# Kernel optimization log

Measured on AMD Instinct MI355X. Metric: run time of the kernel, lower is better.

## Reference

```python
import jax, jax.numpy as jnp
import numpy as np

D_MODEL = 128
N_HEAD = 6
D_HEAD = D_MODEL // N_HEAD  # 21
D_CAT = N_HEAD * D_HEAD     # 126 (note: != d_model, matches torch source)
D_FF = 4 * D_MODEL
EPS = 1e-5


def setup_inputs() -> dict:
    key = jax.random.key(0)
    ks = jax.random.split(key, 12)
    B, T = 512, 128
    s = 0.02
    return {
        "x":  jax.random.normal(ks[0], (B, T, D_MODEL), dtype=jnp.float32),
        "Wq": jax.random.normal(ks[1], (N_HEAD, D_MODEL, D_HEAD), dtype=jnp.float32) * s,
        "Wk": jax.random.normal(ks[2], (N_HEAD, D_MODEL, D_HEAD), dtype=jnp.float32) * s,
        "Wv": jax.random.normal(ks[3], (N_HEAD, D_MODEL, D_HEAD), dtype=jnp.float32) * s,
        "Wo": jax.random.normal(ks[4], (D_CAT, D_MODEL), dtype=jnp.float32) * s,
        "bo": jnp.zeros((D_MODEL,), dtype=jnp.float32),
        "W1": jax.random.normal(ks[5], (D_MODEL, D_FF), dtype=jnp.float32) * s,
        "b1": jnp.zeros((D_FF,), dtype=jnp.float32),
        "W2": jax.random.normal(ks[6], (D_FF, D_MODEL), dtype=jnp.float32) * s,
        "b2": jnp.zeros((D_MODEL,), dtype=jnp.float32),
        "g1": jnp.ones((D_MODEL,), dtype=jnp.float32),
        "beta1": jnp.zeros((D_MODEL,), dtype=jnp.float32),
        "g2": jnp.ones((D_MODEL,), dtype=jnp.float32),
        "beta2": jnp.zeros((D_MODEL,), dtype=jnp.float32),
    }


def _layernorm(x, g, b):
    mu = jnp.mean(x, axis=-1, keepdims=True)
    var = jnp.mean(jnp.square(x - mu), axis=-1, keepdims=True)
    return (x - mu) * jax.lax.rsqrt(var + EPS) * g + b


def reference(x, Wq, Wk, Wv, Wo, bo, W1, b1, W2, b2, g1, beta1, g2, beta2):
    B, T, _ = x.shape
    # --- masked multi-head self-attention on ln1(x) (pre-norm), dropout = eval/identity ---
    h = _layernorm(x, g1, beta1)
    q = jnp.einsum('btd,hde->bhte', h, Wq)
    k = jnp.einsum('btd,hde->bhte', h, Wk)
    v = jnp.einsum('btd,hde->bhte', h, Wv)
    scores = jnp.einsum('bhte,bhse->bhts', q, k) / jnp.sqrt(jnp.float32(D_HEAD))
    causal = jnp.tril(jnp.ones((T, T), dtype=bool))  # tril buffer, T x T
    scores = jnp.where(causal, scores, jnp.float32(-jnp.inf))
    a = jax.nn.softmax(scores, axis=-1)
    o = jnp.einsum('bhts,bhse->bhte', a, v)
    o = o.transpose(0, 2, 1, 3).reshape(B, T, D_CAT)  # concat heads -> 126
    x = x + (o @ Wo + bo)
    # --- feed-forward on ln2(x) ---
    h2 = _layernorm(x, g2, beta2)
    ff = jax.nn.relu(h2 @ W1 + b1) @ W2 + b2
    return x + ff
```

## Files before the change

### kernel.cpp

```cpp
#include <hip/hip_runtime.h>
#include <math.h>

typedef short short8 __attribute__((ext_vector_type(8)));
typedef float f32x4 __attribute__((ext_vector_type(4)));

constexpr int B_ = 512, T_ = 128, D_ = 128, H_ = 6, E_ = 21, DC_ = 126, F_ = 512;
constexpr float EPS_ = 1e-5f;

__device__ __forceinline__ short f2bf(float f) {
    unsigned u = __float_as_uint(f);
    u = (u + 0x7FFFu + ((u >> 16) & 1u)) >> 16;
    return (short)u;
}
__device__ __forceinline__ unsigned pk2(float lo, float hi) {
    return (unsigned)(unsigned short)f2bf(lo) | ((unsigned)(unsigned short)f2bf(hi) << 16);
}
__device__ __forceinline__ f32x4 mfma16(short8 a, short8 b, f32x4 c) {
    return __builtin_amdgcn_mfma_f32_16x16x32_bf16(a, b, c, 0, 0, 0);
}

__global__ __launch_bounds__(256) void prep_kernel(
    const float* __restrict__ Wq, const float* __restrict__ Wk, const float* __restrict__ Wv,
    const float* __restrict__ Wo, const float* __restrict__ W1, const float* __restrict__ W2,
    short* __restrict__ WcatT, short* __restrict__ W1T, short* __restrict__ W2T,
    short* __restrict__ WoT) {
    int idx = blockIdx.x * 256 + threadIdx.x;
    if (idx < 73728) {
        int n = idx >> 7, k = idx & 127;
        int w = (n >= 384) ? 2 : (n >= 192 ? 1 : 0);
        int rem = n - w * 192;
        int hd = rem >> 5, e = rem & 31;
        float v = 0.f;
        if (e < 21) {
            const float* src = (w == 0) ? Wq : (w == 1) ? Wk : Wv;
            v = src[(hd * 128 + k) * 21 + e];
        }
        WcatT[idx] = f2bf(v);
    } else if (idx < 139264) {
        int i = idx - 73728;
        int j = i >> 7, d = i & 127;
        W1T[i] = f2bf(W1[d * 512 + j]);
    } else if (idx < 204800) {
        int i = idx - 139264;
        int d = i >> 9, j = i & 511;
        W2T[i] = f2bf(W2[j * 128 + d]);
    } else if (idx < 221184) {
        int i = idx - 204800;
        int d = i >> 7, c = i & 127;
        WoT[i] = f2bf(c < 126 ? Wo[c * 128 + d] : 0.f);
    }
}

__global__ __launch_bounds__(512) void qkv_kernel(
    const float* __restrict__ x, const float* __restrict__ g1, const float* __restrict__ be1,
    const short* __restrict__ WcatT,
    short* __restrict__ Qg, short* __restrict__ Kg, short* __restrict__ VTg) {
    __shared__ __align__(16) short hA[T_ * D_];
    int b = blockIdx.x, tid = threadIdx.x;
    const f32x4 fzero = {0.f, 0.f, 0.f, 0.f};
    {
        int r = tid >> 2, q = tid & 3;
        const float* xr = x + ((size_t)b * T_ + r) * D_ + q * 32;
        float vals[32];
        float sum = 0.f, sq = 0.f;
        #pragma unroll
        for (int i = 0; i < 8; ++i) {
            f32x4 v4 = *(const f32x4*)(xr + i * 4);
            #pragma unroll
            for (int j = 0; j < 4; ++j) { float vv = v4[j]; vals[i*4+j] = vv; sum += vv; sq += vv*vv; }
        }
        sum += __shfl_xor(sum, 1); sum += __shfl_xor(sum, 2);
        sq  += __shfl_xor(sq, 1);  sq  += __shfl_xor(sq, 2);
        float mu = sum * (1.f / 128.f);
        float rs = rsqrtf(sq * (1.f / 128.f) - mu * mu + EPS_);
        char* hb = (char*)hA;
        #pragma unroll
        for (int cc = 0; cc < 4; ++cc) {
            short8 pk;
            #pragma unroll
            for (int j = 0; j < 8; ++j) {
                int d0 = q * 32 + cc * 8 + j;
                pk[j] = f2bf((vals[cc*8+j] - mu) * rs * g1[d0] + be1[d0]);
            }
            int byte = (r * 256 + q * 64 + cc * 16) ^ ((r & 7) << 4);
            *(short8*)(hb + byte) = pk;
        }
    }
    __syncthreads();
    int lane = tid & 63, wid = tid >> 6;
    int wm = wid >> 2, wn = wid & 3;
    int rlo = lane & 15, khi = lane >> 4;
    f32x4 acc[4][9];
    #pragma unroll
    for (int m = 0; m < 4; ++m)
        #pragma unroll
        for (int j = 0; j < 9; ++j) acc[m][j] = fzero;
    const char* hb = (const char*)hA;
    #pragma unroll
    for (int ks = 0; ks < 4; ++ks) {
        short8 hfr[4];
        #pragma unroll
        for (int m = 0; m < 4; ++m) {
            int row = (wm * 4 + m) * 16 + rlo;
            hfr[m] = *(const short8*)(hb + ((row * 256 + ks * 64 + khi * 16) ^ ((row & 7) << 4)));
        }
        #pragma unroll
        for (int j = 0; j < 9; ++j) {
            int nt = wn * 9 + j;
            short8 wf = *(const short8*)(WcatT + (size_t)(nt * 16 + rlo) * 128 + ks * 32 + khi * 8);
            if (nt < 24) {
                #pragma unroll
                for (int m = 0; m < 4; ++m) acc[m][j] = mfma16(wf, hfr[m], acc[m][j]);
            } else {
                #pragma unroll
                for (int m = 0; m < 4; ++m) acc[m][j] = mfma16(hfr[m], wf, acc[m][j]);
            }
        }
    }
    #pragma unroll
    for (int j = 0; j < 9; ++j) {
        int nt = wn * 9 + j;
        if (nt < 24) {
            int ng = nt * 16 + khi * 4;
            int w = (ng >= 192) ? 1 : 0;
            int hd = (ng >> 5) - w * 6;
            int e32 = ng & 31;
            short* dst = (w ? Kg : Qg) + (((size_t)b * 6 + hd) * 128) * 32 + e32;
            #pragma unroll
            for (int m = 0; m < 4; ++m) {
                int t = (wm * 4 + m) * 16 + rlo;
                uint2 pv;
                pv.x = pk2(acc[m][j][0], acc[m][j][1]);
                pv.y = pk2(acc[m][j][2], acc[m][j][3]);
                *(uint2*)(dst + (size_t)t * 32) = pv;
            }
        } else {
            int ng = nt * 16 + rlo;
            int hd = (ng >> 5) - 12;
            int e32 = ng & 31;
            short* dst = VTg + (((size_t)b * 6 + hd) * 32 + e32) * 128;
            #pragma unroll
            for (int m = 0; m < 4; ++m) {
                int t0 = (wm * 4 + m) * 16 + khi * 4;
                uint2 pv;
                pv.x = pk2(acc[m][j][0], acc[m][j][1]);
                pv.y = pk2(acc[m][j][2], acc[m][j][3]);
                *(uint2*)(dst + t0) = pv;
            }
        }
    }
}

__global__ __launch_bounds__(256) void attn_kernel(
    const short* __restrict__ Qg, const short* __restrict__ Kg, const short* __restrict__ VTg,
    short* __restrict__ Obf) {
    __shared__ __align__(16) short Ks[T_ * 32];
    __shared__ __align__(16) short VTs[32 * T_];
    __shared__ __align__(16) short Ps[T_ * T_];
    int h = blockIdx.x, b = blockIdx.y, tid = threadIdx.x;
    size_t bh = (size_t)b * 6 + h;
    const f32x4 fzero = {0.f, 0.f, 0.f, 0.f};
    {
        char* kb = (char*)Ks;
        const short* Ksrc = Kg + bh * (128 * 32);
        #pragma unroll
        for (int c = tid; c < 512; c += 256) {
            int r = c >> 2, cc = c & 3;
            *(short8*)(kb + ((r * 64 + cc * 16) ^ ((r & 3) << 4))) =
                *(const short8*)(Ksrc + r * 32 + cc * 8);
        }
        char* vb = (char*)VTs;
        const short* Vsrc = VTg + bh * (32 * 128);
        #pragma unroll
        for (int c = tid; c < 512; c += 256) {
            int e = c >> 4, cc = c & 15;
            *(short8*)(vb + ((e * 256 + cc * 16) ^ ((e & 7) << 4))) =
                *(const short8*)(Vsrc + e * 128 + cc * 8);
        }
    }
    __syncthreads();
    int lane = tid & 63, wid = tid >> 6;
    int rlo = lane & 15, khi = lane >> 4;
    const float s2 = 0.31482188f;
    const char* kb = (const char*)Ks;
    const char* vb = (const char*)VTs;
    char* pb = (char*)Ps;
    #pragma unroll
    for (int pass = 0; pass < 2; ++pass) {
        int Mt = (pass == 0) ? wid : 7 - wid;
        int t = Mt * 16 + rlo;
        short8 qf = *(const short8*)(Qg + (bh * 128 + t) * 32 + khi * 8);
        f32x4 sacc[8];
        #pragma unroll
        for (int St = 0; St < 8; ++St) {
            sacc[St] = fzero;
            if (St <= Mt) {
                int srow = St * 16 + rlo;
                short8 kf = *(const short8*)(kb + ((srow * 64 + khi * 16) ^ ((srow & 3) << 4)));
                sacc[St] = mfma16(kf, qf, sacc[St]);
            }
        }
        float m = -3e38f;
        #pragma unroll
        for (int St = 0; St < 8; ++St)
            #pragma unroll
            for (int reg = 0; reg < 4; ++reg) {
                int s = St * 16 + khi * 4 + reg;
                float v = (s <= t) ? sacc[St][reg] * s2 : -3e38f;
                sacc[St][reg] = v;
                m = fmaxf(m, v);
            }
        m = fmaxf(m, __shfl_xor(m, 16));
        m = fmaxf(m, __shfl_xor(m, 32));
        float sum = 0.f;
        #pragma unroll
        for (int St = 0; St < 8; ++St)
            #pragma unroll
            for (int reg = 0; reg < 4; ++reg) {
                float p = exp2f(sacc[St][reg] - m);
                sacc[St][reg] = p;
                sum += p;
            }
        sum += __shfl_xor(sum, 16);
        sum += __shfl_xor(sum, 32);
        float inv = 1.f / sum;
        #pragma unroll
        for (int St = 0; St < 8; ++St) {
            uint2 pv;
            pv.x = pk2(sacc[St][0] * inv, sacc[St][1] * inv);
            pv.y = pk2(sacc[St][2] * inv, sacc[St][3] * inv);
            *(uint2*)(pb + ((t * 256 + St * 32 + khi * 8) ^ ((t & 7) << 4))) = pv;
        }
        f32x4 o0 = fzero, o1 = fzero;
        int kmax = Mt >> 1;
        for (int ks = 0; ks <= kmax; ++ks) {
            int kof = ks * 64 + khi * 16;
            int arow = Mt * 16 + rlo;
            short8 pa = *(const short8*)(pb + ((arow * 256 + kof) ^ ((arow & 7) << 4)));
            short8 b0 = *(const short8*)(vb + ((rlo * 256 + kof) ^ ((rlo & 7) << 4)));
            short8 b1v = *(const short8*)(vb + (((16 + rlo) * 256 + kof) ^ (((16 + rlo) & 7) << 4)));
            o0 = mfma16(pa, b0, o0);
            o1 = mfma16(pa, b1v, o1);
        }
        #pragma unroll
        for (int reg = 0; reg < 4; ++reg) {
            int t2 = Mt * 16 + khi * 4 + reg;
            Obf[((size_t)b * 128 + t2) * 128 + h * 21 + rlo] = f2bf(o0[reg]);
            if (rlo < 5)
                Obf[((size_t)b * 128 + t2) * 128 + h * 21 + 16 + rlo] = f2bf(o1[reg]);
        }
    }
}

__global__ __launch_bounds__(256) void proj_kernel(
    const float* __restrict__ x, const short* __restrict__ Obf, const short* __restrict__ WoT,
    const float* __restrict__ bo, float* __restrict__ out) {
    __shared__ __align__(16) short Os[64 * 128];
    int r0 = blockIdx.x * 64, tid = threadIdx.x;
    const f32x4 fzero = {0.f, 0.f, 0.f, 0.f};
    char* ob = (char*)Os;
    for (int c = tid; c < 1024; c += 256) {
        int r = c >> 4, cc = c & 15;
        short8 v = *(const short8*)(Obf + (size_t)(r0 + r) * 128 + cc * 8);
        if (cc == 15) { v[6] = 0; v[7] = 0; }
        int byte = (r * 256 + cc * 16) ^ ((r & 7) << 4);
        *(short8*)(ob + byte) = v;
    }
    __syncthreads();
    int lane = tid & 63, mt = tid >> 6;
    int rlo = lane & 15, khi = lane >> 4;
    #pragma unroll
    for (int nt = 0; nt < 8; ++nt) {
        int d = nt * 16 + rlo;
        f32x4 acc = fzero;
        #pragma unroll
        for (int ks = 0; ks < 4; ++ks) {
            int arow = mt * 16 + rlo;
            short8 a = *(const short8*)(ob + ((arow * 256 + ks * 64 + khi * 16) ^ ((arow & 7) << 4)));
            short8 bf = *(const short8*)(WoT + d * 128 + ks * 32 + khi * 8);
            acc = mfma16(a, bf, acc);
        }
        float bod = bo[d];
        #pragma unroll
        for (int reg = 0; reg < 4; ++reg) {
            int row = r0 + mt * 16 + khi * 4 + reg;
            out[(size_t)row * 128 + d] = x[(size_t)row * 128 + d] + bod + acc[reg];
        }
    }
}

__global__ __launch_bounds__(256, 2) void ff_kernel(
    float* __restrict__ out, const float* __restrict__ g2, const float* __restrict__ be2,
    const short* __restrict__ W1T, const float* __restrict__ b1,
    const short* __restrict__ W2T, const float* __restrict__ b2) {
    __shared__ __align__(16) short Hs[64 * 128];
    __shared__ __align__(16) short Fs[64 * 512];
    int tid = threadIdx.x;
    int lane = tid & 63, wid = tid >> 6;
    int rlo = lane & 15, khi = lane >> 4;
    int rowbase = blockIdx.x * 64;
    const f32x4 fzero = {0.f, 0.f, 0.f, 0.f};
    {
        int rl = lane >> 2, q = lane & 3;
        int r = wid * 16 + rl;
        const float* xr = out + (size_t)(rowbase + r) * D_ + q * 32;
        float vals[32];
        float sum = 0.f, sq = 0.f;
        #pragma unroll
        for (int i = 0; i < 8; ++i) {
            f32x4 v4 = *(const f32x4*)(xr + i * 4);
            #pragma unroll
            for (int j = 0; j < 4; ++j) { float vv = v4[j]; vals[i*4+j] = vv; sum += vv; sq += vv*vv; }
        }
        sum += __shfl_xor(sum, 1); sum += __shfl_xor(sum, 2);
        sq  += __shfl_xor(sq, 1);  sq  += __shfl_xor(sq, 2);
        float mu = sum * (1.f / 128.f);
        float rs = rsqrtf(sq * (1.f / 128.f) - mu * mu + EPS_);
        char* hb = (char*)Hs;
        #pragma unroll
        for (int cc = 0; cc < 4; ++cc) {
            short8 pk;
            #pragma unroll
            for (int j = 0; j < 8; ++j) {
                int d0 = q * 32 + cc * 8 + j;
                pk[j] = f2bf((vals[cc*8+j] - mu) * rs * g2[d0] + be2[d0]);
            }
            int byte = (r * 256 + q * 64 + cc * 16) ^ ((r & 7) << 4);
            *(short8*)(hb + byte) = pk;
        }
    }
    __syncthreads();
    short8 hfr[4][4];
    {
        const char* hb = (const char*)Hs;
        #pragma unroll
        for (int mt = 0; mt < 4; ++mt)
            #pragma unroll
            for (int kk = 0; kk < 4; ++kk) {
                int t = mt * 16 + rlo;
                hfr[mt][kk] = *(const short8*)(hb + ((t * 256 + kk * 64 + khi * 16) ^ ((t & 7) << 4)));
            }
    }
    {
        const short* W1w = W1T + (size_t)(wid * 128) * 128;
        char* fb = (char*)Fs;
        #pragma unroll 2
        for (int jt = 0; jt < 8; ++jt) {
            f32x4 fa[4];
            #pragma unroll
            for (int mt = 0; mt < 4; ++mt) fa[mt] = fzero;
            #pragma unroll
            for (int kk = 0; kk < 4; ++kk) {
                short8 wa = *(const short8*)(W1w + (size_t)(jt * 16 + rlo) * 128 + kk * 32 + khi * 8);
                #pragma unroll
                for (int mt = 0; mt < 4; ++mt) fa[mt] = mfma16(wa, hfr[mt][kk], fa[mt]);
            }
            f32x4 bq = *(const f32x4*)(b1 + wid * 128 + jt * 16 + khi * 4);
            #pragma unroll
            for (int mt = 0; mt < 4; ++mt) {
                float v0 = fmaxf(fa[mt][0] + bq[0], 0.f);
                float v1 = fmaxf(fa[mt][1] + bq[1], 0.f);
                float v2 = fmaxf(fa[mt][2] + bq[2], 0.f);
                float v3 = fmaxf(fa[mt][3] + bq[3], 0.f);
                uint2 w;
                w.x = pk2(v0, v1);
                w.y = pk2(v2, v3);
                int t = mt * 16 + rlo;
                int byte = (t * 1024 + wid * 256 + jt * 32 + khi * 8) ^ ((t & 7) << 4);
                *(uint2*)(fb + byte) = w;
            }
        }
    }
    __syncthreads();
    f32x4 oa[4][2];
    #pragma unroll
    for (int mt = 0; mt < 4; ++mt) { oa[mt][0] = fzero; oa[mt][1] = fzero; }
    {
        const char* fb = (const char*)Fs;
        const short* W2w = W2T + (size_t)(wid * 32) * 512;
        #pragma unroll 4
        for (int ks = 0; ks < 16; ++ks) {
            short8 af[4];
            #pragma unroll
            for (int mt = 0; mt < 4; ++mt) {
                int t = mt * 16 + rlo;
                af[mt] = *(const short8*)(fb + ((t * 1024 + ks * 64 + khi * 16) ^ ((t & 7) << 4)));
            }
            #pragma unroll
            for (int nd = 0; nd < 2; ++nd) {
                short8 wf = *(const short8*)(W2w + (size_t)(nd * 16 + rlo) * 512 + ks * 32 + khi * 8);
                #pragma unroll
                for (int mt = 0; mt < 4; ++mt) oa[mt][nd] = mfma16(af[mt], wf, oa[mt][nd]);
            }
        }
    }
    #pragma unroll
    for (int nd = 0; nd < 2; ++nd) {
        int d = wid * 32 + nd * 16 + rlo;
        float b2d = b2[d];
        #pragma unroll
        for (int mt = 0; mt < 4; ++mt) {
            #pragma unroll
            for (int reg = 0; reg < 4; ++reg) {
                int row = rowbase + mt * 16 + khi * 4 + reg;
                size_t gi = (size_t)row * D_ + d;
                out[gi] = out[gi] + b2d + oa[mt][nd][reg];
            }
        }
    }
}

extern "C" void kernel_launch(void* const* d_in, const int* in_sizes, int n_in,
                              void* d_out, int out_size, void* d_ws, size_t ws_size,
                              hipStream_t stream) {
    const float* x   = (const float*)d_in[0];
    const float* Wq  = (const float*)d_in[1];
    const float* Wk  = (const float*)d_in[2];
    const float* Wv  = (const float*)d_in[3];
    const float* Wo  = (const float*)d_in[4];
    const float* bo  = (const float*)d_in[5];
    const float* W1  = (const float*)d_in[6];
    const float* b1  = (const float*)d_in[7];
    const float* W2  = (const float*)d_in[8];
    const float* b2  = (const float*)d_in[9];
    const float* g1  = (const float*)d_in[10];
    const float* be1 = (const float*)d_in[11];
    const float* g2  = (const float*)d_in[12];
    const float* be2 = (const float*)d_in[13];
    float* out = (float*)d_out;

    char* wsb = (char*)d_ws;
    short* WcatT = (short*)(wsb);
    short* W1T   = (short*)(wsb + 147456);
    short* W2T   = (short*)(wsb + 278528);
    short* WoT   = (short*)(wsb + 409600);
    short* Qg    = (short*)(wsb + 442368);
    short* Kg    = (short*)(wsb + 25608192);
    short* VTg   = (short*)(wsb + 50774016);
    short* Obf   = (short*)(wsb + 75939840);

    prep_kernel<<<864, 256, 0, stream>>>(Wq, Wk, Wv, Wo, W1, W2, WcatT, W1T, W2T, WoT);
    qkv_kernel<<<512, 512, 0, stream>>>(x, g1, be1, WcatT, Qg, Kg, VTg);
    attn_kernel<<<dim3(6, 512), 256, 0, stream>>>(Qg, Kg, VTg, Obf);
    proj_kernel<<<1024, 256, 0, stream>>>(x, Obf, WoT, bo, out);
    ff_kernel<<<1024, 256, 0, stream>>>(out, g2, be2, W1T, b1, W2T, b2);
}
```

Before: 283.5 us.

## Fuse QKV projection, attention and output projection into one per-batch kernel

Merges the QKV, attention and projection kernels into a single kernel per batch element. Q, K, V^T and the concatenated head outputs stay in shared memory, and heads are processed sequentially with block-wide syncs. This removes the large bf16 intermediate round trips through global memory and two kernel launches. In exchange, LDS use grows to about 120KB per block, which limits occupancy to one 512-thread block per CU and serializes heads within a block.

```diff
diff --git a/kernel.cpp b/kernel.cpp
--- a/kernel.cpp
+++ b/kernel.cpp
@@ -51,11 +51,16 @@
     }
 }
 
-__global__ __launch_bounds__(512) void qkv_kernel(
+__global__ __launch_bounds__(512, 2) void mega_kernel(
     const float* __restrict__ x, const float* __restrict__ g1, const float* __restrict__ be1,
-    const short* __restrict__ WcatT,
-    short* __restrict__ Qg, short* __restrict__ Kg, short* __restrict__ VTg) {
+    const short* __restrict__ WcatT, const short* __restrict__ WoT,
+    const float* __restrict__ bo, float* __restrict__ out) {
     __shared__ __align__(16) short hA[T_ * D_];
+    __shared__ __align__(16) short Qh[T_ * 32];
+    __shared__ __align__(16) short Kh[T_ * 32];
+    __shared__ __align__(16) short VTh[32 * T_];
+    __shared__ __align__(16) short Ps[T_ * T_];
+    __shared__ __align__(16) short Os[T_ * T_];
     int b = blockIdx.x, tid = threadIdx.x;
     const f32x4 fzero = {0.f, 0.f, 0.f, 0.f};
     {
@@ -85,206 +90,153 @@
             int byte = (r * 256 + q * 64 + cc * 16) ^ ((r & 7) << 4);
             *(short8*)(hb + byte) = pk;
         }
-    }
-    __syncthreads();
-    int lane = tid & 63, wid = tid >> 6;
-    int wm = wid >> 2, wn = wid & 3;
-    int rlo = lane & 15, khi = lane >> 4;
-    f32x4 acc[4][9];
-    #pragma unroll
-    for (int m = 0; m < 4; ++m)
-        #pragma unroll
-        for (int j = 0; j < 9; ++j) acc[m][j] = fzero;
-    const char* hb = (const char*)hA;
-    #pragma unroll
-    for (int ks = 0; ks < 4; ++ks) {
-        short8 hfr[4];
-        #pragma unroll
-        for (int m = 0; m < 4; ++m) {
-            int row = (wm * 4 + m) * 16 + rlo;
-            hfr[m] = *(const short8*)(hb + ((row * 256 + ks * 64 + khi * 16) ^ ((row & 7) << 4)));
-        }
-        #pragma unroll
-        for (int j = 0; j < 9; ++j) {
-            int nt = wn * 9 + j;
-            short8 wf = *(const short8*)(WcatT + (size_t)(nt * 16 + rlo) * 128 + ks * 32 + khi * 8);
-            if (nt < 24) {
-                #pragma unroll
-                for (int m = 0; m < 4; ++m) acc[m][j] = mfma16(wf, hfr[m], acc[m][j]);
-            } else {
-                #pragma unroll
-                for (int m = 0; m < 4; ++m) acc[m][j] = mfma16(hfr[m], wf, acc[m][j]);
-            }
-        }
-    }
-    #pragma unroll
-    for (int j = 0; j < 9; ++j) {
-        int nt = wn * 9 + j;
-        if (nt < 24) {
-            int ng = nt * 16 + khi * 4;
-            int w = (ng >= 192) ? 1 : 0;
-            int hd = (ng >> 5) - w * 6;
-            int e32 = ng & 31;
-            short* dst = (w ? Kg : Qg) + (((size_t)b * 6 + hd) * 128) * 32 + e32;
-            #pragma unroll
-            for (int m = 0; m < 4; ++m) {
-                int t = (wm * 4 + m) * 16 + rlo;
-                uint2 pv;
-                pv.x = pk2(acc[m][j][0], acc[m][j][1]);
-                pv.y = pk2(acc[m][j][2], acc[m][j][3]);
-                *(uint2*)(dst + (size_t)t * 32) = pv;
-            }
-        } else {
-            int ng = nt * 16 + rlo;
-            int hd = (ng >> 5) - 12;
-            int e32 = ng & 31;
-            short* dst = VTg + (((size_t)b * 6 + hd) * 32 + e32) * 128;
-            #pragma unroll
-            for (int m = 0; m < 4; ++m) {
-                int t0 = (wm * 4 + m) * 16 + khi * 4;
-                uint2 pv;
-                pv.x = pk2(acc[m][j][0], acc[m][j][1]);
-                pv.y = pk2(acc[m][j][2], acc[m][j][3]);
-                *(uint2*)(dst + t0) = pv;
-            }
-        }
-    }
-}
-
-__global__ __launch_bounds__(256) void attn_kernel(
-    const short* __restrict__ Qg, const short* __restrict__ Kg, const short* __restrict__ VTg,
-    short* __restrict__ Obf) {
-    __shared__ __align__(16) short Ks[T_ * 32];
-    __shared__ __align__(16) short VTs[32 * T_];
-    __shared__ __align__(16) short Ps[T_ * T_];
-    int h = blockIdx.x, b = blockIdx.y, tid = threadIdx.x;
-    size_t bh = (size_t)b * 6 + h;
-    const f32x4 fzero = {0.f, 0.f, 0.f, 0.f};
-    {
-        char* kb = (char*)Ks;
-        const short* Ksrc = Kg + bh * (128 * 32);
-        #pragma unroll
-        for (int c = tid; c < 512; c += 256) {
-            int r = c >> 2, cc = c & 3;
-            *(short8*)(kb + ((r * 64 + cc * 16) ^ ((r & 3) << 4))) =
-                *(const short8*)(Ksrc + r * 32 + cc * 8);
-        }
-        char* vb = (char*)VTs;
-        const short* Vsrc = VTg + bh * (32 * 128);
-        #pragma unroll
-        for (int c = tid; c < 512; c += 256) {
-            int e = c >> 4, cc = c & 15;
-            *(short8*)(vb + ((e * 256 + cc * 16) ^ ((e & 7) << 4))) =
-                *(const short8*)(Vsrc + e * 128 + cc * 8);
-        }
+        short8 z = {0,0,0,0,0,0,0,0};
+        char* ob = (char*)Os;
+        #pragma unroll
+        for (int i = tid; i < 2048; i += 512) *(short8*)(ob + i * 16) = z;
     }
     __syncthreads();
     int lane = tid & 63, wid = tid >> 6;
     int rlo = lane & 15, khi = lane >> 4;
+    short8 hfr[4];
+    {
+        const char* hb = (const char*)hA;
+        int row = wid * 16 + rlo;
+        #pragma unroll
+        for (int kk = 0; kk < 4; ++kk)
+            hfr[kk] = *(const short8*)(hb + ((row * 256 + kk * 64 + khi * 16) ^ ((row & 7) << 4)));
+    }
     const float s2 = 0.31482188f;
-    const char* kb = (const char*)Ks;
-    const char* vb = (const char*)VTs;
+    char* qhb = (char*)Qh;
+    char* khb = (char*)Kh;
+    char* vtb = (char*)VTh;
     char* pb = (char*)Ps;
-    #pragma unroll
-    for (int pass = 0; pass < 2; ++pass) {
-        int Mt = (pass == 0) ? wid : 7 - wid;
-        int t = Mt * 16 + rlo;
-        short8 qf = *(const short8*)(Qg + (bh * 128 + t) * 32 + khi * 8);
-        f32x4 sacc[8];
-        #pragma unroll
-        for (int St = 0; St < 8; ++St) {
-            sacc[St] = fzero;
-            if (St <= Mt) {
-                int srow = St * 16 + rlo;
-                short8 kf = *(const short8*)(kb + ((srow * 64 + khi * 16) ^ ((srow & 3) << 4)));
-                sacc[St] = mfma16(kf, qf, sacc[St]);
-            }
-        }
-        float m = -3e38f;
-        #pragma unroll
-        for (int St = 0; St < 8; ++St)
+    char* osb = (char*)Os;
+    for (int h = 0; h < 6; ++h) {
+        const short* Wqb = WcatT + (size_t)(h * 32) * 128;
+        const short* Wkb = WcatT + (size_t)(192 + h * 32) * 128;
+        const short* Wvb = WcatT + (size_t)(384 + h * 32) * 128;
+        #pragma unroll
+        for (int nq = 0; nq < 2; ++nq) {
+            f32x4 qa = fzero, ka = fzero;
+            #pragma unroll
+            for (int ks = 0; ks < 4; ++ks) {
+                short8 wfq = *(const short8*)(Wqb + (size_t)(nq * 16 + rlo) * 128 + ks * 32 + khi * 8);
+                short8 wfk = *(const short8*)(Wkb + (size_t)(nq * 16 + rlo) * 128 + ks * 32 + khi * 8);
+                qa = mfma16(wfq, hfr[ks], qa);
+                ka = mfma16(wfk, hfr[ks], ka);
+            }
+            int t = wid * 16 + rlo;
+            int byte = (t * 64 + (nq * 16 + khi * 4) * 2) ^ ((t & 3) << 4);
+            uint2 qv, kv;
+            qv.x = pk2(qa[0], qa[1]); qv.y = pk2(qa[2], qa[3]);
+            kv.x = pk2(ka[0], ka[1]); kv.y = pk2(ka[2], ka[3]);
+            *(uint2*)(qhb + byte) = qv;
+            *(uint2*)(khb + byte) = kv;
+        }
+        #pragma unroll
+        for (int nv = 0; nv < 2; ++nv) {
+            f32x4 va = fzero;
+            #pragma unroll
+            for (int ks = 0; ks < 4; ++ks) {
+                short8 wfv = *(const short8*)(Wvb + (size_t)(nv * 16 + rlo) * 128 + ks * 32 + khi * 8);
+                va = mfma16(hfr[ks], wfv, va);
+            }
+            int e = nv * 16 + rlo;
+            int t0 = wid * 16 + khi * 4;
+            int byte = (e * 256 + t0 * 2) ^ ((e & 7) << 4);
+            uint2 vv;
+            vv.x = pk2(va[0], va[1]); vv.y = pk2(va[2], va[3]);
+            *(uint2*)(vtb + byte) = vv;
+        }
+        __syncthreads();
+        #pragma unroll
+        for (int pass = 0; pass < 2; ++pass) {
+            int Mt = (pass == 0) ? wid : 7 - wid;
+            int t = Mt * 16 + rlo;
+            short8 qf = *(const short8*)(qhb + ((t * 64 + khi * 16) ^ ((t & 3) << 4)));
+            f32x4 sacc[8];
+            #pragma unroll
+            for (int St = 0; St < 8; ++St) {
+                sacc[St] = fzero;
+                if (St <= Mt) {
+                    int srow = St * 16 + rlo;
+                    short8 kf = *(const short8*)(khb + ((srow * 64 + khi * 16) ^ ((srow & 3) << 4)));
+                    sacc[St] = mfma16(kf, qf, sacc[St]);
+                }
+            }
+            float m = -3e38f;
+            #pragma unroll
+            for (int St = 0; St < 8; ++St)
+                #pragma unroll
+                for (int reg = 0; reg < 4; ++reg) {
+                    int s = St * 16 + khi * 4 + reg;
+                    float v = (s <= t) ? sacc[St][reg] * s2 : -3e38f;
+                    sacc[St][reg] = v;
+                    m = fmaxf(m, v);
+                }
+            m = fmaxf(m, __shfl_xor(m, 16));
+            m = fmaxf(m, __shfl_xor(m, 32));
+            float sum = 0.f;
+            #pragma unroll
+            for (int St = 0; St < 8; ++St)
+                #pragma unroll
+                for (int reg = 0; reg < 4; ++reg) {
+                    float p = exp2f(sacc[St][reg] - m);
+                    sacc[St][reg] = p;
+                    sum += p;
+                }
+            sum += __shfl_xor(sum, 16);
+            sum += __shfl_xor(sum, 32);
+            float inv = 1.f / sum;
+            #pragma unroll
+            for (int St = 0; St < 8; ++St) {
+                uint2 pv;
+                pv.x = pk2(sacc[St][0] * inv, sacc[St][1] * inv);
+                pv.y = pk2(sacc[St][2] * inv, sacc[St][3] * inv);
+                *(uint2*)(pb + ((t * 256 + St * 32 + khi * 8) ^ ((t & 7) << 4))) = pv;
+            }
+            f32x4 o0 = fzero, o1 = fzero;
+            int kmax = Mt >> 1;
+            for (int ks = 0; ks <= kmax; ++ks) {
+                int kof = ks * 64 + khi * 16;
+                int arow = Mt * 16 + rlo;
+                short8 pa = *(const short8*)(pb + ((arow * 256 + kof) ^ ((arow & 7) << 4)));
+                short8 b0 = *(const short8*)(vtb + ((rlo * 256 + kof) ^ ((rlo & 7) << 4)));
+                short8 b1v = *(const short8*)(vtb + (((16 + rlo) * 256 + kof) ^ (((16 + rlo) & 7) << 4)));
+                o0 = mfma16(pa, b0, o0);
+                o1 = mfma16(pa, b1v, o1);
+            }
             #pragma unroll
             for (int reg = 0; reg < 4; ++reg) {
-                int s = St * 16 + khi * 4 + reg;
-                float v = (s <= t) ? sacc[St][reg] * s2 : -3e38f;
-                sacc[St][reg] = v;
-                m = fmaxf(m, v);
-            }
-        m = fmaxf(m, __shfl_xor(m, 16));
-        m = fmaxf(m, __shfl_xor(m, 32));
-        float sum = 0.f;
-        #pragma unroll
-        for (int St = 0; St < 8; ++St)
-            #pragma unroll
-            for (int reg = 0; reg < 4; ++reg) {
-                float p = exp2f(sacc[St][reg] - m);
-                sacc[St][reg] = p;
-                sum += p;
-            }
-        sum += __shfl_xor(sum, 16);
-        sum += __shfl_xor(sum, 32);
-        float inv = 1.f / sum;
-        #pragma unroll
-        for (int St = 0; St < 8; ++St) {
-            uint2 pv;
-            pv.x = pk2(sacc[St][0] * inv, sacc[St][1] * inv);
-            pv.y = pk2(sacc[St][2] * inv, sacc[St][3] * inv);
-            *(uint2*)(pb + ((t * 256 + St * 32 + khi * 8) ^ ((t & 7) << 4))) = pv;
-        }
-        f32x4 o0 = fzero, o1 = fzero;
-        int kmax = Mt >> 1;
-        for (int ks = 0; ks <= kmax; ++ks) {
-            int kof = ks * 64 + khi * 16;
-            int arow = Mt * 16 + rlo;
-            short8 pa = *(const short8*)(pb + ((arow * 256 + kof) ^ ((arow & 7) << 4)));
-            short8 b0 = *(const short8*)(vb + ((rlo * 256 + kof) ^ ((rlo & 7) << 4)));
-            short8 b1v = *(const short8*)(vb + (((16 + rlo) * 256 + kof) ^ (((16 + rlo) & 7) << 4)));
-            o0 = mfma16(pa, b0, o0);
-            o1 = mfma16(pa, b1v, o1);
-        }
-        #pragma unroll
-        for (int reg = 0; reg < 4; ++reg) {
-            int t2 = Mt * 16 + khi * 4 + reg;
-            Obf[((size_t)b * 128 + t2) * 128 + h * 21 + rlo] = f2bf(o0[reg]);
-            if (rlo < 5)
-                Obf[((size_t)b * 128 + t2) * 128 + h * 21 + 16 + rlo] = f2bf(o1[reg]);
-        }
-    }
-}
-
-__global__ __launch_bounds__(256) void proj_kernel(
-    const float* __restrict__ x, const short* __restrict__ Obf, const short* __restrict__ WoT,
-    const float* __restrict__ bo, float* __restrict__ out) {
-    __shared__ __align__(16) short Os[64 * 128];
-    int r0 = blockIdx.x * 64, tid = threadIdx.x;
-    const f32x4 fzero = {0.f, 0.f, 0.f, 0.f};
-    char* ob = (char*)Os;
-    for (int c = tid; c < 1024; c += 256) {
-        int r = c >> 4, cc = c & 15;
-        short8 v = *(const short8*)(Obf + (size_t)(r0 + r) * 128 + cc * 8);
-        if (cc == 15) { v[6] = 0; v[7] = 0; }
-        int byte = (r * 256 + cc * 16) ^ ((r & 7) << 4);
-        *(short8*)(ob + byte) = v;
-    }
-    __syncthreads();
-    int lane = tid & 63, mt = tid >> 6;
-    int rlo = lane & 15, khi = lane >> 4;
+                int t2 = Mt * 16 + khi * 4 + reg;
+                int col = h * 21 + rlo;
+                *(short*)(osb + ((t2 * 256 + col * 2) ^ ((t2 & 7) << 4))) = f2bf(o0[reg]);
+                if (rlo < 5) {
+                    int col1 = h * 21 + 16 + rlo;
+                    *(short*)(osb + ((t2 * 256 + col1 * 2) ^ ((t2 & 7) << 4))) = f2bf(o1[reg]);
+                }
+            }
+        }
+        __syncthreads();
+    }
     #pragma unroll
     for (int nt = 0; nt < 8; ++nt) {
         int d = nt * 16 + rlo;
         f32x4 acc = fzero;
         #pragma unroll
         for (int ks = 0; ks < 4; ++ks) {
-            int arow = mt * 16 + rlo;
-            short8 a = *(const short8*)(ob + ((arow * 256 + ks * 64 + khi * 16) ^ ((arow & 7) << 4)));
-            short8 bf = *(const short8*)(WoT + d * 128 + ks * 32 + khi * 8);
+            int arow = wid * 16 + rlo;
+            short8 a = *(const short8*)(osb + ((arow * 256 + ks * 64 + khi * 16) ^ ((arow & 7) << 4)));
+            short8 bf = *(const short8*)(WoT + (size_t)d * 128 + ks * 32 + khi * 8);
             acc = mfma16(a, bf, acc);
         }
         float bod = bo[d];
         #pragma unroll
         for (int reg = 0; reg < 4; ++reg) {
-            int row = r0 + mt * 16 + khi * 4 + reg;
-            out[(size_t)row * 128 + d] = x[(size_t)row * 128 + d] + bod + acc[reg];
+            int row = wid * 16 + khi * 4 + reg;
+            size_t gi = ((size_t)b * T_ + row) * D_ + d;
+            out[gi] = x[gi] + bod + acc[reg];
         }
     }
 }
@@ -434,14 +386,8 @@
     short* W1T   = (short*)(wsb + 147456);
     short* W2T   = (short*)(wsb + 278528);
     short* WoT   = (short*)(wsb + 409600);
-    short* Qg    = (short*)(wsb + 442368);
-    short* Kg    = (short*)(wsb + 25608192);
-    short* VTg   = (short*)(wsb + 50774016);
-    short* Obf   = (short*)(wsb + 75939840);
 
     prep_kernel<<<864, 256, 0, stream>>>(Wq, Wk, Wv, Wo, W1, W2, WcatT, W1T, W2T, WoT);
-    qkv_kernel<<<512, 512, 0, stream>>>(x, g1, be1, WcatT, Qg, Kg, VTg);
-    attn_kernel<<<dim3(6, 512), 256, 0, stream>>>(Qg, Kg, VTg, Obf);
-    proj_kernel<<<1024, 256, 0, stream>>>(x, Obf, WoT, bo, out);
+    mega_kernel<<<512, 512, 0, stream>>>(x, g1, be1, WcatT, WoT, bo, out);
     ff_kernel<<<1024, 256, 0, stream>>>(out, g2, be2, W1T, b1, W2T, b2);
 }
```

Measured after the change: 312.5 us. 1.1x slower.

## Split QKV kernel into 32-row blocks and skip padded head-dim traffic

Applied to the files above, without the earlier changes.

The QKV projection kernel now launches four 256-thread blocks per batch, each covering 32 rows, instead of one 512-thread block per batch. Each warp preloads its LDS fragments once and handles 9 output column tiles for 2 row tiles. The QKV kernel also stops writing the padded head-dim lanes (e 24..31), and the attention kernel stops reading them, filling zeros in LDS instead. The aim is more blocks for better occupancy and less global memory traffic, at the cost of reading the weight fragments more times overall.

```diff
diff --git a/kernel.cpp b/kernel.cpp
--- a/kernel.cpp
+++ b/kernel.cpp
@@ -51,101 +51,111 @@
     }
 }
 
-__global__ __launch_bounds__(512) void qkv_kernel(
+__global__ __launch_bounds__(256) void qkv_kernel(
     const float* __restrict__ x, const float* __restrict__ g1, const float* __restrict__ be1,
     const short* __restrict__ WcatT,
     short* __restrict__ Qg, short* __restrict__ Kg, short* __restrict__ VTg) {
-    __shared__ __align__(16) short hA[T_ * D_];
-    int b = blockIdx.x, tid = threadIdx.x;
+    __shared__ __align__(16) short hA[32 * 128];
+    int bid = blockIdx.x;
+    int b = bid >> 2, r0 = (bid & 3) * 32;
+    int tid = threadIdx.x;
     const f32x4 fzero = {0.f, 0.f, 0.f, 0.f};
     {
-        int r = tid >> 2, q = tid & 3;
-        const float* xr = x + ((size_t)b * T_ + r) * D_ + q * 32;
-        float vals[32];
+        int r = tid >> 3, q = tid & 7;
+        const float* xr = x + ((size_t)b * T_ + r0 + r) * D_ + q * 16;
+        float vals[16];
         float sum = 0.f, sq = 0.f;
         #pragma unroll
-        for (int i = 0; i < 8; ++i) {
+        for (int i = 0; i < 4; ++i) {
             f32x4 v4 = *(const f32x4*)(xr + i * 4);
             #pragma unroll
             for (int j = 0; j < 4; ++j) { float vv = v4[j]; vals[i*4+j] = vv; sum += vv; sq += vv*vv; }
         }
-        sum += __shfl_xor(sum, 1); sum += __shfl_xor(sum, 2);
-        sq  += __shfl_xor(sq, 1);  sq  += __shfl_xor(sq, 2);
+        sum += __shfl_xor(sum, 1); sum += __shfl_xor(sum, 2); sum += __shfl_xor(sum, 4);
+        sq  += __shfl_xor(sq, 1);  sq  += __shfl_xor(sq, 2);  sq  += __shfl_xor(sq, 4);
         float mu = sum * (1.f / 128.f);
         float rs = rsqrtf(sq * (1.f / 128.f) - mu * mu + EPS_);
         char* hb = (char*)hA;
         #pragma unroll
-        for (int cc = 0; cc < 4; ++cc) {
+        for (int cc = 0; cc < 2; ++cc) {
             short8 pk;
             #pragma unroll
             for (int j = 0; j < 8; ++j) {
-                int d0 = q * 32 + cc * 8 + j;
+                int d0 = q * 16 + cc * 8 + j;
                 pk[j] = f2bf((vals[cc*8+j] - mu) * rs * g1[d0] + be1[d0]);
             }
-            int byte = (r * 256 + q * 64 + cc * 16) ^ ((r & 7) << 4);
+            int byte = (r * 256 + q * 32 + cc * 16) ^ ((r & 7) << 4);
             *(short8*)(hb + byte) = pk;
         }
     }
     __syncthreads();
     int lane = tid & 63, wid = tid >> 6;
-    int wm = wid >> 2, wn = wid & 3;
     int rlo = lane & 15, khi = lane >> 4;
-    f32x4 acc[4][9];
-    #pragma unroll
-    for (int m = 0; m < 4; ++m)
+    short8 hfr[2][4];
+    {
+        const char* hb = (const char*)hA;
+        #pragma unroll
+        for (int m = 0; m < 2; ++m)
+            #pragma unroll
+            for (int kk = 0; kk < 4; ++kk) {
+                int row = m * 16 + rlo;
+                hfr[m][kk] = *(const short8*)(hb + ((row * 256 + kk * 64 + khi * 16) ^ ((row & 7) << 4)));
+            }
+    }
+    f32x4 acc[2][9];
+    #pragma unroll
+    for (int m = 0; m < 2; ++m)
         #pragma unroll
         for (int j = 0; j < 9; ++j) acc[m][j] = fzero;
-    const char* hb = (const char*)hA;
     #pragma unroll
     for (int ks = 0; ks < 4; ++ks) {
-        short8 hfr[4];
-        #pragma unroll
-        for (int m = 0; m < 4; ++m) {
-            int row = (wm * 4 + m) * 16 + rlo;
-            hfr[m] = *(const short8*)(hb + ((row * 256 + ks * 64 + khi * 16) ^ ((row & 7) << 4)));
-        }
         #pragma unroll
         for (int j = 0; j < 9; ++j) {
-            int nt = wn * 9 + j;
+            int nt = wid * 9 + j;
             short8 wf = *(const short8*)(WcatT + (size_t)(nt * 16 + rlo) * 128 + ks * 32 + khi * 8);
             if (nt < 24) {
                 #pragma unroll
-                for (int m = 0; m < 4; ++m) acc[m][j] = mfma16(wf, hfr[m], acc[m][j]);
+                for (int m = 0; m < 2; ++m) acc[m][j] = mfma16(wf, hfr[m][ks], acc[m][j]);
             } else {
                 #pragma unroll
-                for (int m = 0; m < 4; ++m) acc[m][j] = mfma16(hfr[m], wf, acc[m][j]);
+                for (int m = 0; m < 2; ++m) acc[m][j] = mfma16(hfr[m][ks], wf, acc[m][j]);
             }
         }
     }
     #pragma unroll
     for (int j = 0; j < 9; ++j) {
-        int nt = wn * 9 + j;
+        int nt = wid * 9 + j;
+        bool odd = (nt & 1) != 0;
         if (nt < 24) {
             int ng = nt * 16 + khi * 4;
             int w = (ng >= 192) ? 1 : 0;
             int hd = (ng >> 5) - w * 6;
             int e32 = ng & 31;
-            short* dst = (w ? Kg : Qg) + (((size_t)b * 6 + hd) * 128) * 32 + e32;
-            #pragma unroll
-            for (int m = 0; m < 4; ++m) {
-                int t = (wm * 4 + m) * 16 + rlo;
-                uint2 pv;
-                pv.x = pk2(acc[m][j][0], acc[m][j][1]);
-                pv.y = pk2(acc[m][j][2], acc[m][j][3]);
-                *(uint2*)(dst + (size_t)t * 32) = pv;
+            if (!(odd && khi >= 2)) {
+                short* dst = (w ? Kg : Qg) + (((size_t)b * 6 + hd) * 128) * 32 + e32;
+                #pragma unroll
+                for (int m = 0; m < 2; ++m) {
+                    int t = r0 + m * 16 + rlo;
+                    uint2 pv;
+                    pv.x = pk2(acc[m][j][0], acc[m][j][1]);
+                    pv.y = pk2(acc[m][j][2], acc[m][j][3]);
+                    *(uint2*)(dst + (size_t)t * 32) = pv;
+                }
             }
         } else {
             int ng = nt * 16 + rlo;
             int hd = (ng >> 5) - 12;
             int e32 = ng & 31;
-            short* dst = VTg + (((size_t)b * 6 + hd) * 32 + e32) * 128;
-            #pragma unroll
-            for (int m = 0; m < 4; ++m) {
-                int t0 = (wm * 4 + m) * 16 + khi * 4;
-                uint2 pv;
-                pv.x = pk2(acc[m][j][0], acc[m][j][1]);
-                pv.y = pk2(acc[m][j][2], acc[m][j][3]);
-                *(uint2*)(dst + t0) = pv;
+            if (!(odd && rlo >= 8)) {
+                short* dst = VTg + (((size_t)b * 6 + hd) * 32 + e32) * 128;
+                #pragma unroll
+                for (int m = 0; m < 2; ++m) {
+                    int t0 = r0 + m * 16 + khi * 4;
+                    uint2 pv;
+                    pv.x = pk2(acc[m][j][0], acc[m][j][1]);
+                    pv.y = pk2(acc[m][j][2], acc[m][j][3]);
+                    *(uint2*)(dst + t0) = pv;
+                }
             }
         }
     }
@@ -163,19 +173,20 @@
     {
         char* kb = (char*)Ks;
         const short* Ksrc = Kg + bh * (128 * 32);
+        const short8 z8 = {0,0,0,0,0,0,0,0};
         #pragma unroll
         for (int c = tid; c < 512; c += 256) {
             int r = c >> 2, cc = c & 3;
-            *(short8*)(kb + ((r * 64 + cc * 16) ^ ((r & 3) << 4))) =
-                *(const short8*)(Ksrc + r * 32 + cc * 8);
+            short8 kv = (cc < 3) ? *(const short8*)(Ksrc + r * 32 + cc * 8) : z8;
+            *(short8*)(kb + ((r * 64 + cc * 16) ^ ((r & 3) << 4))) = kv;
         }
         char* vb = (char*)VTs;
         const short* Vsrc = VTg + bh * (32 * 128);
         #pragma unroll
         for (int c = tid; c < 512; c += 256) {
             int e = c >> 4, cc = c & 15;
-            *(short8*)(vb + ((e * 256 + cc * 16) ^ ((e & 7) << 4))) =
-                *(const short8*)(Vsrc + e * 128 + cc * 8);
+            short8 vv = (e < 24) ? *(const short8*)(Vsrc + e * 128 + cc * 8) : z8;
+            *(short8*)(vb + ((e * 256 + cc * 16) ^ ((e & 7) << 4))) = vv;
         }
     }
     __syncthreads();
@@ -277,7 +288,7 @@
         for (int ks = 0; ks < 4; ++ks) {
             int arow = mt * 16 + rlo;
             short8 a = *(const short8*)(ob + ((arow * 256 + ks * 64 + khi * 16) ^ ((arow & 7) << 4)));
-            short8 bf = *(const short8*)(WoT + d * 128 + ks * 32 + khi * 8);
+            short8 bf = *(const short8*)(WoT + (size_t)d * 128 + ks * 32 + khi * 8);
             acc = mfma16(a, bf, acc);
         }
         float bod = bo[d];
@@ -440,7 +451,7 @@
     short* Obf   = (short*)(wsb + 75939840);
 
     prep_kernel<<<864, 256, 0, stream>>>(Wq, Wk, Wv, Wo, W1, W2, WcatT, W1T, W2T, WoT);
-    qkv_kernel<<<512, 512, 0, stream>>>(x, g1, be1, WcatT, Qg, Kg, VTg);
+    qkv_kernel<<<2048, 256, 0, stream>>>(x, g1, be1, WcatT, Qg, Kg, VTg);
     attn_kernel<<<dim3(6, 512), 256, 0, stream>>>(Qg, Kg, VTg, Obf);
     proj_kernel<<<1024, 256, 0, stream>>>(x, Obf, WoT, bo, out);
     ff_kernel<<<1024, 256, 0, stream>>>(out, g2, be2, W1T, b1, W2T, b2);
```

After: 267.2 us. -5.7%, faster.
